# Optimization experiments

Hardware: AMD Instinct MI355X
Metric: run time of the kernel (lower is better)

## Reference

```python
import jax, jax.numpy as jnp
import numpy as np
import math

DIM = 384
HEADS = 12
WIN = (12, 12)
N = WIN[0] * WIN[1]  # 144
TABLE = (2 * WIN[0] - 1) * (2 * WIN[1] - 1)  # 529
B_ = 512
NW = 16
CPB_HIDDEN = 512


def setup_inputs() -> dict:
    key = jax.random.key(0)
    ks = jax.random.split(key, 12)
    x = jax.random.normal(ks[0], (B_, N, DIM), dtype=jnp.float32)
    relative_coords_table = jax.random.uniform(ks[1], (1, 2 * WIN[0] - 1, 2 * WIN[1] - 1, 2), dtype=jnp.float32) * 2.0 - 1.0
    relative_position_index = jax.random.randint(ks[2], (N, N), 0, TABLE, dtype=jnp.int64)
    mask = jnp.zeros((NW, N, N), dtype=jnp.float32)
    # learned params
    qkv_w = jax.random.normal(ks[3], (3 * DIM, DIM), dtype=jnp.float32) * (1.0 / math.sqrt(DIM))
    q_bias = jnp.zeros((DIM,), dtype=jnp.float32)
    k_bias = jnp.zeros((DIM,), dtype=jnp.float32)
    v_bias = jnp.zeros((DIM,), dtype=jnp.float32)
    logit_scale = jnp.full((HEADS, 1, 1), math.log(10.0), dtype=jnp.float32)
    cpb_w1 = jax.random.normal(ks[4], (CPB_HIDDEN, 2), dtype=jnp.float32) * 0.5
    cpb_b1 = jnp.zeros((CPB_HIDDEN,), dtype=jnp.float32)
    cpb_w2 = jax.random.normal(ks[5], (HEADS, CPB_HIDDEN), dtype=jnp.float32) * (1.0 / math.sqrt(CPB_HIDDEN))
    proj_w = jax.random.normal(ks[6], (DIM, DIM), dtype=jnp.float32) * (1.0 / math.sqrt(DIM))
    proj_b = jnp.zeros((DIM,), dtype=jnp.float32)
    return {
        'x': x,
        'relative_coords_table': relative_coords_table,
        'relative_position_index': relative_position_index,
        'mask': mask,
        'qkv_w': qkv_w, 'q_bias': q_bias, 'k_bias': k_bias, 'v_bias': v_bias,
        'logit_scale': logit_scale,
        'cpb_w1': cpb_w1, 'cpb_b1': cpb_b1, 'cpb_w2': cpb_w2,
        'proj_w': proj_w, 'proj_b': proj_b,
    }


def reference(x, relative_coords_table, relative_position_index, mask,
              qkv_w, q_bias, k_bias, v_bias, logit_scale,
              cpb_w1, cpb_b1, cpb_w2, proj_w, proj_b):
    Bw, n, C = x.shape
    H = HEADS
    d = C // H
    qkv_bias = jnp.concatenate([q_bias, k_bias, v_bias])
    qkv = x @ qkv_w.T + qkv_bias  # (Bw, n, 3C)
    qkv = qkv.reshape(Bw, n, 3, H, d).transpose(2, 0, 3, 1, 4)  # (3, Bw, H, n, d)
    q, k, v = qkv[0], qkv[1], qkv[2]
    # cosine attention
    qn = q / jnp.linalg.norm(q, axis=-1, keepdims=True)
    kn = k / jnp.linalg.norm(k, axis=-1, keepdims=True)
    attn = jnp.einsum('bhnd,bhmd->bhnm', qn, kn)
    scale = jnp.exp(jnp.minimum(logit_scale, math.log(1.0 / 0.01)))  # (H,1,1)
    attn = attn * scale[None]
    # CPB-MLP relative position bias
    h1 = jax.nn.relu(relative_coords_table @ cpb_w1.T + cpb_b1)  # (1,23,23,512)
    table = (h1 @ cpb_w2.T).reshape(-1, H)  # (529, H)
    rpb = table[relative_position_index.reshape(-1)].reshape(n, n, H)
    rpb = 16.0 * jax.nn.sigmoid(rpb.transpose(2, 0, 1))  # (H, n, n)
    attn = attn + rpb[None]
    # shifted-window mask
    nW = mask.shape[0]
    attn = attn.reshape(Bw // nW, nW, H, n, n) + mask[None, :, None]
    attn = attn.reshape(Bw, H, n, n)
    attn = jax.nn.softmax(attn, axis=-1)
    out = jnp.einsum('bhnm,bhmd->bhnd', attn, v)
    out = out.transpose(0, 2, 1, 3).reshape(Bw, n, C)
    out = out @ proj_w.T + proj_b
    return out
```

## Files before the change

kernel.cpp:

```cpp
#include <hip/hip_runtime.h>

#define DIMC 384
#define NHEADS 12
#define NTOK 144
#define TABLEN 529
#define BWIN 512
#define NWIN 16
#define CPBH 512

typedef unsigned short u16;
typedef unsigned int u32;
typedef __attribute__((ext_vector_type(8))) short short8;
typedef __attribute__((ext_vector_type(4))) float f32x4;

#define MFMA(a, b, c) __builtin_amdgcn_mfma_f32_16x16x32_bf16((a), (b), (c), 0, 0, 0)

__device__ __forceinline__ u16 f2bf(float f) {
  union { float f; u32 u; } v; v.f = f;
  u32 r = v.u + 0x7fffu + ((v.u >> 16) & 1u);
  return (u16)(r >> 16);
}
__device__ __forceinline__ u32 pk2(float a, float b) {
  return (u32)f2bf(a) | ((u32)f2bf(b) << 16);
}

__global__ __launch_bounds__(256) void cvt_bf16(const float* __restrict__ in,
                                                u16* __restrict__ out, int n8) {
  int i = blockIdx.x * 256 + threadIdx.x;
  if (i >= n8) return;
  const float4* p = (const float4*)(in + (size_t)i * 8);
  float4 a = p[0], b = p[1];
  uint4 r;
  r.x = pk2(a.x, a.y); r.y = pk2(a.z, a.w);
  r.z = pk2(b.x, b.y); r.w = pk2(b.z, b.w);
  *(uint4*)(out + (size_t)i * 8) = r;
}

__global__ void cpb_kernel(const float* __restrict__ rct,
                           const float* __restrict__ w1,
                           const float* __restrict__ b1,
                           const float* __restrict__ w2,
                           const float* __restrict__ logit_scale,
                           float* __restrict__ bias_tab,
                           float* __restrict__ scalev) {
  int t = blockIdx.x * blockDim.x + threadIdx.x;
  if (t < NHEADS) scalev[t] = __expf(fminf(logit_scale[t], 4.60517018598809f));
  if (t >= TABLEN * NHEADS) return;
  int i = t / NHEADS, h = t % NHEADS;
  float c0 = rct[2 * i], c1 = rct[2 * i + 1];
  const float* w2h = w2 + (size_t)h * CPBH;
  float acc = 0.f;
  for (int k = 0; k < CPBH; ++k) {
    float hv = fmaxf(0.f, fmaf(c0, w1[2 * k], fmaf(c1, w1[2 * k + 1], b1[k])));
    acc = fmaf(hv, w2h[k], acc);
  }
  bias_tab[i * NHEADS + h] = 16.f / (1.f + __expf(-acc));
}

__global__ __launch_bounds__(256) void cbias_kernel(const int* __restrict__ rpi,
                                                    const float* __restrict__ bias_tab,
                                                    const float* __restrict__ mask,
                                                    float* __restrict__ cb) {
  int e = blockIdx.x * 256 + threadIdx.x;
  if (e >= NWIN * NHEADS * NTOK * NTOK) return;
  int m = e % NTOK;
  int t = e / NTOK;
  int n = t % NTOK; t /= NTOK;
  int h = t % NHEADS;
  int w = t / NHEADS;
  cb[e] = bias_tab[rpi[n * NTOK + m] * NHEADS + h] + mask[(w * NTOK + n) * NTOK + m];
}

__global__ __launch_bounds__(576) void attn_fused(
    const u16* __restrict__ xb, const u16* __restrict__ wb,
    const float* __restrict__ q_bias, const float* __restrict__ k_bias,
    const float* __restrict__ v_bias, const float* __restrict__ cb,
    const float* __restrict__ scalev, u16* __restrict__ ctx) {
  __shared__ u16 smem[22656];
  u16* qn = smem;
  u16* kn = smem + 5760;
  u16* vT = smem + 11520;
  u16* Pc = smem + 16896;
  u16* xs = smem;
  u16* wsm = smem + 9216;

  int bid = blockIdx.x;
  int xcd = bid & 7;
  int i = bid >> 3;
  int wsub = i / 384;
  int j = i - wsub * 384;
  int bI = j / NHEADS;
  int h = j - bI * NHEADS;
  int w = xcd * 2 + wsub;
  int b = bI * NWIN + w;

  int tid = threadIdx.x;
  int lane = tid & 63, wv = tid >> 6;
  int g = lane >> 4, c = lane & 15;
  int rbase = wv * 16;

  f32x4 acc[6];
#pragma unroll
  for (int d = 0; d < 6; ++d) acc[d] = (f32x4){0.f, 0.f, 0.f, 0.f};

  int r4 = tid >> 2, b4 = tid & 3;
  bool hasW = tid < 384;
  int wrow = (r4 >> 5) * DIMC + h * 32 + (r4 & 31);
  int xwo0 = r4 * 64 + 8 * (b4 ^ (r4 & 7));
  int xwo1 = r4 * 64 + 8 * ((b4 + 4) ^ (r4 & 7));

  uint4 px, pw;
  px = *(const uint4*)(xb + ((size_t)b * NTOK + r4) * DIMC + b4 * 8);
  if (hasW) pw = *(const uint4*)(wb + (size_t)wrow * DIMC + b4 * 8);

  for (int t = 0; t < 12; ++t) {
    int xwo = (t & 1) ? xwo1 : xwo0;
    *(uint4*)(xs + xwo) = px;
    if (hasW) *(uint4*)(wsm + xwo) = pw;
    __syncthreads();
    if (t < 11) {
      int k0 = (t + 1) * 32;
      px = *(const uint4*)(xb + ((size_t)b * NTOK + r4) * DIMC + k0 + b4 * 8);
      if (hasW) pw = *(const uint4*)(wb + (size_t)wrow * DIMC + k0 + b4 * 8);
    }
    int par4 = (t & 1) * 4;
    int arow = rbase + c;
    short8 ax = *(const short8*)(xs + arow * 64 + 8 * ((g + par4) ^ (arow & 7)));
#pragma unroll
    for (int ni = 0; ni < 6; ++ni) {
      int row = ni * 16 + c;
      short8 bw = *(const short8*)(wsm + row * 64 + 8 * ((g + par4) ^ (row & 7)));
      acc[ni] = MFMA(ax, bw, acc[ni]);
    }
  }
  __syncthreads();

  float sch = scalev[h];
  float qb0 = q_bias[h * 32 + c], qb1 = q_bias[h * 32 + 16 + c];
  float kb0 = k_bias[h * 32 + c], kb1 = k_bias[h * 32 + 16 + c];
  float vb0 = v_bias[h * 32 + c], vb1 = v_bias[h * 32 + 16 + c];
#pragma unroll
  for (int r = 0; r < 4; ++r) {
    int row = rbase + g * 4 + r;
    float q0 = acc[0][r] + qb0, q1 = acc[1][r] + qb1;
    float ssq = q0 * q0 + q1 * q1;
    ssq += __shfl_xor(ssq, 1); ssq += __shfl_xor(ssq, 2);
    ssq += __shfl_xor(ssq, 4); ssq += __shfl_xor(ssq, 8);
    float siq = sch / sqrtf(ssq);
    qn[row * 40 + c] = f2bf(q0 * siq);
    qn[row * 40 + 16 + c] = f2bf(q1 * siq);
    float k0v = acc[2][r] + kb0, k1v = acc[3][r] + kb1;
    float ssk = k0v * k0v + k1v * k1v;
    ssk += __shfl_xor(ssk, 1); ssk += __shfl_xor(ssk, 2);
    ssk += __shfl_xor(ssk, 4); ssk += __shfl_xor(ssk, 8);
    float sik = 1.f / sqrtf(ssk);
    kn[row * 40 + c] = f2bf(k0v * sik);
    kn[row * 40 + 16 + c] = f2bf(k1v * sik);
    float v0 = acc[4][r] + vb0;
    float v1 = acc[5][r] + vb1;
    vT[c * 168 + row] = f2bf(v0);
    vT[(16 + c) * 168 + row] = f2bf(v1);
  }
  if (tid < 32) {
    uint4 z4 = {0u, 0u, 0u, 0u};
    *(uint4*)(vT + tid * 168 + 144) = z4;
    *(uint4*)(vT + tid * 168 + 152) = z4;
    *(uint4*)(vT + tid * 168 + 160) = z4;
  }
  __syncthreads();

  short8 aq = *(const short8*)(qn + (rbase + c) * 40 + g * 8);
  f32x4 S[9];
#pragma unroll
  for (int mt = 0; mt < 9; ++mt) {
    short8 bk = *(const short8*)(kn + (mt * 16 + c) * 40 + g * 8);
    f32x4 z = (f32x4){0.f, 0.f, 0.f, 0.f};
    S[mt] = MFMA(aq, bk, z);
  }

  const float* cbh = cb + (((size_t)w * NHEADS + h) * NTOK) * NTOK;
#pragma unroll
  for (int r = 0; r < 4; ++r) {
    int row = rbase + g * 4 + r;
    const float* crow = cbh + (size_t)row * NTOK + c;
    float sv[9];
    float mx = -1e30f;
#pragma unroll
    for (int mt = 0; mt < 9; ++mt) {
      float s = S[mt][r] + crow[mt * 16];
      sv[mt] = s;
      mx = fmaxf(mx, s);
    }
    mx = fmaxf(mx, __shfl_xor(mx, 1)); mx = fmaxf(mx, __shfl_xor(mx, 2));
    mx = fmaxf(mx, __shfl_xor(mx, 4)); mx = fmaxf(mx, __shfl_xor(mx, 8));
    float sum = 0.f;
#pragma unroll
    for (int mt = 0; mt < 9; ++mt) {
      float p = __expf(sv[mt] - mx);
      sv[mt] = p;
      sum += p;
    }
    sum += __shfl_xor(sum, 1); sum += __shfl_xor(sum, 2);
    sum += __shfl_xor(sum, 4); sum += __shfl_xor(sum, 8);
    float rinv = 1.f / sum;
#pragma unroll
    for (int mt = 0; mt < 9; ++mt) S[mt][r] = sv[mt] * rinv;
  }

  f32x4 po[2];
  po[0] = (f32x4){0.f, 0.f, 0.f, 0.f};
  po[1] = (f32x4){0.f, 0.f, 0.f, 0.f};
  for (int ck = 0; ck < 5; ++ck) {
#pragma unroll
    for (int mt2 = 0; mt2 < 2; ++mt2) {
      int MT = ck * 2 + mt2;
#pragma unroll
      for (int r = 0; r < 4; ++r) {
        int row = rbase + g * 4 + r;
        float p = (MT < 9) ? S[MT][r] : 0.f;
        Pc[row * 40 + mt2 * 16 + c] = f2bf(p);
      }
    }
    short8 pa = *(const short8*)(Pc + (rbase + c) * 40 + g * 8);
#pragma unroll
    for (int dt = 0; dt < 2; ++dt) {
      short8 vb = *(const short8*)(vT + (dt * 16 + c) * 168 + ck * 32 + g * 8);
      po[dt] = MFMA(pa, vb, po[dt]);
    }
  }

#pragma unroll
  for (int dt = 0; dt < 2; ++dt)
#pragma unroll
    for (int r = 0; r < 4; ++r) {
      int n = rbase + g * 4 + r;
      ctx[((size_t)b * NTOK + n) * DIMC + h * 32 + dt * 16 + c] = f2bf(po[dt][r]);
    }
}

__global__ __launch_bounds__(256) void proj_gemm(const u16* __restrict__ ctx,
                                                 const u16* __restrict__ pwb,
                                                 const float* __restrict__ proj_b,
                                                 float* __restrict__ out) {
  __shared__ u16 As[128 * 64];
  __shared__ u16 Bs[128 * 64];
  int bid = blockIdx.x;
  int nblk = bid % 3, mblk = bid / 3;
  size_t gm0 = (size_t)mblk * 128;
  int gn0 = nblk * 128;
  int tid = threadIdx.x, lane = tid & 63, wid = tid >> 6;
  int wr = wid >> 1, wc = wid & 1, g = lane >> 4, c = lane & 15;
  f32x4 acc[4][4];
#pragma unroll
  for (int i = 0; i < 4; ++i)
#pragma unroll
    for (int j = 0; j < 4; ++j) acc[i][j] = (f32x4){0.f, 0.f, 0.f, 0.f};

  for (int t = 0; t < 6; ++t) {
    int k0 = t * 64;
#pragma unroll
    for (int p = 0; p < 4; ++p) {
      int row = p * 32 + (tid >> 3);
      int seg = (tid & 7) * 8;
      uint4 va = *(const uint4*)(ctx + (gm0 + row) * DIMC + k0 + seg);
      *(uint4*)(As + row * 64 + seg) = va;
      uint4 vb = *(const uint4*)(pwb + (size_t)(gn0 + row) * DIMC + k0 + seg);
      *(uint4*)(Bs + row * 64 + seg) = vb;
    }
    __syncthreads();
#pragma unroll
    for (int kk = 0; kk < 64; kk += 32) {
      short8 a[4], bfr[4];
#pragma unroll
      for (int mi = 0; mi < 4; ++mi)
        a[mi] = *(const short8*)(As + (wr * 64 + mi * 16 + c) * 64 + kk + g * 8);
#pragma unroll
      for (int ni = 0; ni < 4; ++ni)
        bfr[ni] = *(const short8*)(Bs + (wc * 64 + ni * 16 + c) * 64 + kk + g * 8);
#pragma unroll
      for (int mi = 0; mi < 4; ++mi)
#pragma unroll
        for (int ni = 0; ni < 4; ++ni)
          acc[mi][ni] = MFMA(a[mi], bfr[ni], acc[mi][ni]);
    }
    __syncthreads();
  }
#pragma unroll
  for (int mi = 0; mi < 4; ++mi)
#pragma unroll
    for (int ni = 0; ni < 4; ++ni) {
      int gcol = gn0 + wc * 64 + ni * 16 + c;
      float bv = proj_b[gcol];
#pragma unroll
      for (int r = 0; r < 4; ++r) {
        size_t grow = gm0 + wr * 64 + mi * 16 + g * 4 + r;
        out[grow * DIMC + gcol] = acc[mi][ni][r] + bv;
      }
    }
}

extern "C" void kernel_launch(void* const* d_in, const int* in_sizes, int n_in,
                              void* d_out, int out_size, void* d_ws, size_t ws_size,
                              hipStream_t stream) {
  const float* x = (const float*)d_in[0];
  const float* rct = (const float*)d_in[1];
  const int* rpi = (const int*)d_in[2];
  const float* mask = (const float*)d_in[3];
  const float* qkv_w = (const float*)d_in[4];
  const float* q_bias = (const float*)d_in[5];
  const float* k_bias = (const float*)d_in[6];
  const float* v_bias = (const float*)d_in[7];
  const float* logit_scale = (const float*)d_in[8];
  const float* cpb_w1 = (const float*)d_in[9];
  const float* cpb_b1 = (const float*)d_in[10];
  const float* cpb_w2 = (const float*)d_in[11];
  const float* proj_w = (const float*)d_in[12];
  const float* proj_b = (const float*)d_in[13];
  float* out = (float*)d_out;

  char* ws = (char*)d_ws;
  size_t off = 0;
  auto alloc = [&](size_t bytes) {
    void* p = ws + off;
    off = (off + bytes + 255) & ~(size_t)255;
    return p;
  };
  const size_t NX = (size_t)BWIN * NTOK * DIMC;
  u16* xb = (u16*)alloc(NX * 2);
  u16* wqb = (u16*)alloc((size_t)3 * DIMC * DIMC * 2);
  u16* pwb = (u16*)alloc((size_t)DIMC * DIMC * 2);
  u16* ctx = (u16*)alloc(NX * 2);
  float* cbv = (float*)alloc((size_t)NWIN * NHEADS * NTOK * NTOK * 4);
  float* bias_tab = (float*)alloc((size_t)TABLEN * NHEADS * 4);
  float* scalev = (float*)alloc(64 * 4);

  cvt_bf16<<<(int)(NX / 8 + 255) / 256, 256, 0, stream>>>(x, xb, (int)(NX / 8));
  cvt_bf16<<<(3 * DIMC * DIMC / 8 + 255) / 256, 256, 0, stream>>>(qkv_w, wqb, 3 * DIMC * DIMC / 8);
  cvt_bf16<<<(DIMC * DIMC / 8 + 255) / 256, 256, 0, stream>>>(proj_w, pwb, DIMC * DIMC / 8);
  cpb_kernel<<<(TABLEN * NHEADS + 255) / 256, 256, 0, stream>>>(
      rct, cpb_w1, cpb_b1, cpb_w2, logit_scale, bias_tab, scalev);
  cbias_kernel<<<(NWIN * NHEADS * NTOK * NTOK + 255) / 256, 256, 0, stream>>>(
      rpi, bias_tab, mask, cbv);
  attn_fused<<<BWIN * NHEADS, 576, 0, stream>>>(
      xb, wqb, q_bias, k_bias, v_bias, cbv, scalev, ctx);
  proj_gemm<<<(BWIN * NTOK / 128) * 3, 256, 0, stream>>>(ctx, pwb, proj_b, out);
}
```

Before: 350.2 us.

## Process two heads per attention block to reuse loaded x tiles

Each attention block now computes the QKV projection for two heads at once, sharing each staged x tile across twice as many weight rows. The softmax attention for the two heads then runs sequentially inside the block. This halves the grid and cuts redundant x reads from global memory and L2. In exchange it raises accumulator register pressure, adds an extra barrier, and gives fewer, longer blocks.

```diff
diff --git a/kernel.cpp b/kernel.cpp
--- a/kernel.cpp
+++ b/kernel.cpp
@@ -87,155 +87,178 @@
   int bid = blockIdx.x;
   int xcd = bid & 7;
   int i = bid >> 3;
-  int wsub = i / 384;
-  int j = i - wsub * 384;
-  int bI = j / NHEADS;
-  int h = j - bI * NHEADS;
+  int wsub = i / 192;
+  int j = i - wsub * 192;
+  int bI = j / 6;
+  int hp = j - bI * 6;
   int w = xcd * 2 + wsub;
   int b = bI * NWIN + w;
+  int h0 = hp * 2;
 
   int tid = threadIdx.x;
   int lane = tid & 63, wv = tid >> 6;
   int g = lane >> 4, c = lane & 15;
   int rbase = wv * 16;
 
-  f32x4 acc[6];
-#pragma unroll
-  for (int d = 0; d < 6; ++d) acc[d] = (f32x4){0.f, 0.f, 0.f, 0.f};
+  f32x4 acc[2][6];
+#pragma unroll
+  for (int hh = 0; hh < 2; ++hh)
+#pragma unroll
+    for (int d = 0; d < 6; ++d) acc[hh][d] = (f32x4){0.f, 0.f, 0.f, 0.f};
 
   int r4 = tid >> 2, b4 = tid & 3;
-  bool hasW = tid < 384;
-  int wrow = (r4 >> 5) * DIMC + h * 32 + (r4 & 31);
-  int xwo0 = r4 * 64 + 8 * (b4 ^ (r4 & 7));
-  int xwo1 = r4 * 64 + 8 * ((b4 + 4) ^ (r4 & 7));
-
-  uint4 px, pw;
+  bool hasW1 = tid < 192;
+  int wr1 = 144 + r4;
+  int wg0 = (r4 >> 6) * DIMC + (h0 + ((r4 >> 5) & 1)) * 32 + (r4 & 31);
+  int wg1 = (wr1 >> 6) * DIMC + (h0 + ((wr1 >> 5) & 1)) * 32 + (wr1 & 31);
+  int xo0 = r4 * 64 + 8 * (b4 ^ (r4 & 7));
+  int xo1 = r4 * 64 + 8 * ((b4 + 4) ^ (r4 & 7));
+  int w1o0 = wr1 * 64 + 8 * (b4 ^ (wr1 & 7));
+  int w1o1 = wr1 * 64 + 8 * ((b4 + 4) ^ (wr1 & 7));
+
+  uint4 px, pw0, pw1;
   px = *(const uint4*)(xb + ((size_t)b * NTOK + r4) * DIMC + b4 * 8);
-  if (hasW) pw = *(const uint4*)(wb + (size_t)wrow * DIMC + b4 * 8);
+  pw0 = *(const uint4*)(wb + (size_t)wg0 * DIMC + b4 * 8);
+  if (hasW1) pw1 = *(const uint4*)(wb + (size_t)wg1 * DIMC + b4 * 8);
 
   for (int t = 0; t < 12; ++t) {
-    int xwo = (t & 1) ? xwo1 : xwo0;
-    *(uint4*)(xs + xwo) = px;
-    if (hasW) *(uint4*)(wsm + xwo) = pw;
+    if (t & 1) {
+      *(uint4*)(xs + xo1) = px;
+      *(uint4*)(wsm + xo1) = pw0;
+      if (hasW1) *(uint4*)(wsm + w1o1) = pw1;
+    } else {
+      *(uint4*)(xs + xo0) = px;
+      *(uint4*)(wsm + xo0) = pw0;
+      if (hasW1) *(uint4*)(wsm + w1o0) = pw1;
+    }
     __syncthreads();
     if (t < 11) {
       int k0 = (t + 1) * 32;
       px = *(const uint4*)(xb + ((size_t)b * NTOK + r4) * DIMC + k0 + b4 * 8);
-      if (hasW) pw = *(const uint4*)(wb + (size_t)wrow * DIMC + k0 + b4 * 8);
+      pw0 = *(const uint4*)(wb + (size_t)wg0 * DIMC + k0 + b4 * 8);
+      if (hasW1) pw1 = *(const uint4*)(wb + (size_t)wg1 * DIMC + k0 + b4 * 8);
     }
     int par4 = (t & 1) * 4;
     int arow = rbase + c;
     short8 ax = *(const short8*)(xs + arow * 64 + 8 * ((g + par4) ^ (arow & 7)));
 #pragma unroll
-    for (int ni = 0; ni < 6; ++ni) {
-      int row = ni * 16 + c;
-      short8 bw = *(const short8*)(wsm + row * 64 + 8 * ((g + par4) ^ (row & 7)));
-      acc[ni] = MFMA(ax, bw, acc[ni]);
-    }
+    for (int hh = 0; hh < 2; ++hh)
+#pragma unroll
+      for (int d = 0; d < 6; ++d) {
+        int row = (d >> 1) * 64 + hh * 32 + (d & 1) * 16 + c;
+        short8 bw = *(const short8*)(wsm + row * 64 + 8 * ((g + par4) ^ (row & 7)));
+        acc[hh][d] = MFMA(ax, bw, acc[hh][d]);
+      }
   }
   __syncthreads();
 
-  float sch = scalev[h];
-  float qb0 = q_bias[h * 32 + c], qb1 = q_bias[h * 32 + 16 + c];
-  float kb0 = k_bias[h * 32 + c], kb1 = k_bias[h * 32 + 16 + c];
-  float vb0 = v_bias[h * 32 + c], vb1 = v_bias[h * 32 + 16 + c];
-#pragma unroll
-  for (int r = 0; r < 4; ++r) {
-    int row = rbase + g * 4 + r;
-    float q0 = acc[0][r] + qb0, q1 = acc[1][r] + qb1;
-    float ssq = q0 * q0 + q1 * q1;
-    ssq += __shfl_xor(ssq, 1); ssq += __shfl_xor(ssq, 2);
-    ssq += __shfl_xor(ssq, 4); ssq += __shfl_xor(ssq, 8);
-    float siq = sch / sqrtf(ssq);
-    qn[row * 40 + c] = f2bf(q0 * siq);
-    qn[row * 40 + 16 + c] = f2bf(q1 * siq);
-    float k0v = acc[2][r] + kb0, k1v = acc[3][r] + kb1;
-    float ssk = k0v * k0v + k1v * k1v;
-    ssk += __shfl_xor(ssk, 1); ssk += __shfl_xor(ssk, 2);
-    ssk += __shfl_xor(ssk, 4); ssk += __shfl_xor(ssk, 8);
-    float sik = 1.f / sqrtf(ssk);
-    kn[row * 40 + c] = f2bf(k0v * sik);
-    kn[row * 40 + 16 + c] = f2bf(k1v * sik);
-    float v0 = acc[4][r] + vb0;
-    float v1 = acc[5][r] + vb1;
-    vT[c * 168 + row] = f2bf(v0);
-    vT[(16 + c) * 168 + row] = f2bf(v1);
+#pragma unroll
+  for (int hh = 0; hh < 2; ++hh) {
+    int h = h0 + hh;
+    if (hh) __syncthreads();
+
+    float sch = scalev[h];
+    float qb0 = q_bias[h * 32 + c], qb1 = q_bias[h * 32 + 16 + c];
+    float kb0 = k_bias[h * 32 + c], kb1 = k_bias[h * 32 + 16 + c];
+    float vb0 = v_bias[h * 32 + c], vb1 = v_bias[h * 32 + 16 + c];
+#pragma unroll
+    for (int r = 0; r < 4; ++r) {
+      int row = rbase + g * 4 + r;
+      float q0 = acc[hh][0][r] + qb0, q1 = acc[hh][1][r] + qb1;
+      float ssq = q0 * q0 + q1 * q1;
+      ssq += __shfl_xor(ssq, 1); ssq += __shfl_xor(ssq, 2);
+      ssq += __shfl_xor(ssq, 4); ssq += __shfl_xor(ssq, 8);
+      float siq = sch / sqrtf(ssq);
+      qn[row * 40 + c] = f2bf(q0 * siq);
+      qn[row * 40 + 16 + c] = f2bf(q1 * siq);
+      float k0v = acc[hh][2][r] + kb0, k1v = acc[hh][3][r] + kb1;
+      float ssk = k0v * k0v + k1v * k1v;
+      ssk += __shfl_xor(ssk, 1); ssk += __shfl_xor(ssk, 2);
+      ssk += __shfl_xor(ssk, 4); ssk += __shfl_xor(ssk, 8);
+      float sik = 1.f / sqrtf(ssk);
+      kn[row * 40 + c] = f2bf(k0v * sik);
+      kn[row * 40 + 16 + c] = f2bf(k1v * sik);
+      float v0 = acc[hh][4][r] + vb0;
+      float v1 = acc[hh][5][r] + vb1;
+      vT[c * 168 + row] = f2bf(v0);
+      vT[(16 + c) * 168 + row] = f2bf(v1);
+    }
+    if (hh == 0 && tid < 32) {
+      uint4 z4 = {0u, 0u, 0u, 0u};
+      *(uint4*)(vT + tid * 168 + 144) = z4;
+      *(uint4*)(vT + tid * 168 + 152) = z4;
+      *(uint4*)(vT + tid * 168 + 160) = z4;
+    }
+    __syncthreads();
+
+    short8 aq = *(const short8*)(qn + (rbase + c) * 40 + g * 8);
+    f32x4 S[9];
+#pragma unroll
+    for (int mt = 0; mt < 9; ++mt) {
+      short8 bk = *(const short8*)(kn + (mt * 16 + c) * 40 + g * 8);
+      f32x4 z = (f32x4){0.f, 0.f, 0.f, 0.f};
+      S[mt] = MFMA(aq, bk, z);
+    }
+
+    const float* cbh = cb + (((size_t)w * NHEADS + h) * NTOK) * NTOK;
+#pragma unroll
+    for (int r = 0; r < 4; ++r) {
+      int row = rbase + g * 4 + r;
+      const float* crow = cbh + (size_t)row * NTOK + c;
+      float sv[9];
+      float mx = -1e30f;
+#pragma unroll
+      for (int mt = 0; mt < 9; ++mt) {
+        float s = S[mt][r] + crow[mt * 16];
+        sv[mt] = s;
+        mx = fmaxf(mx, s);
+      }
+      mx = fmaxf(mx, __shfl_xor(mx, 1)); mx = fmaxf(mx, __shfl_xor(mx, 2));
+      mx = fmaxf(mx, __shfl_xor(mx, 4)); mx = fmaxf(mx, __shfl_xor(mx, 8));
+      float sum = 0.f;
+#pragma unroll
+      for (int mt = 0; mt < 9; ++mt) {
+        float p = __expf(sv[mt] - mx);
+        sv[mt] = p;
+        sum += p;
+      }
+      sum += __shfl_xor(sum, 1); sum += __shfl_xor(sum, 2);
+      sum += __shfl_xor(sum, 4); sum += __shfl_xor(sum, 8);
+      float rinv = 1.f / sum;
+#pragma unroll
+      for (int mt = 0; mt < 9; ++mt) S[mt][r] = sv[mt] * rinv;
+    }
+
+    f32x4 po[2];
+    po[0] = (f32x4){0.f, 0.f, 0.f, 0.f};
+    po[1] = (f32x4){0.f, 0.f, 0.f, 0.f};
+    for (int ck = 0; ck < 5; ++ck) {
+#pragma unroll
+      for (int mt2 = 0; mt2 < 2; ++mt2) {
+        int MT = ck * 2 + mt2;
+#pragma unroll
+        for (int r = 0; r < 4; ++r) {
+          int row = rbase + g * 4 + r;
+          float p = (MT < 9) ? S[MT][r] : 0.f;
+          Pc[row * 40 + mt2 * 16 + c] = f2bf(p);
+        }
+      }
+      short8 pa = *(const short8*)(Pc + (rbase + c) * 40 + g * 8);
+#pragma unroll
+      for (int dt = 0; dt < 2; ++dt) {
+        short8 vb = *(const short8*)(vT + (dt * 16 + c) * 168 + ck * 32 + g * 8);
+        po[dt] = MFMA(pa, vb, po[dt]);
+      }
+    }
+
+#pragma unroll
+    for (int dt = 0; dt < 2; ++dt)
+#pragma unroll
+      for (int r = 0; r < 4; ++r) {
+        int n = rbase + g * 4 + r;
+        ctx[((size_t)b * NTOK + n) * DIMC + h * 32 + dt * 16 + c] = f2bf(po[dt][r]);
+      }
   }
-  if (tid < 32) {
-    uint4 z4 = {0u, 0u, 0u, 0u};
-    *(uint4*)(vT + tid * 168 + 144) = z4;
-    *(uint4*)(vT + tid * 168 + 152) = z4;
-    *(uint4*)(vT + tid * 168 + 160) = z4;
-  }
-  __syncthreads();
-
-  short8 aq = *(const short8*)(qn + (rbase + c) * 40 + g * 8);
-  f32x4 S[9];
-#pragma unroll
-  for (int mt = 0; mt < 9; ++mt) {
-    short8 bk = *(const short8*)(kn + (mt * 16 + c) * 40 + g * 8);
-    f32x4 z = (f32x4){0.f, 0.f, 0.f, 0.f};
-    S[mt] = MFMA(aq, bk, z);
-  }
-
-  const float* cbh = cb + (((size_t)w * NHEADS + h) * NTOK) * NTOK;
-#pragma unroll
-  for (int r = 0; r < 4; ++r) {
-    int row = rbase + g * 4 + r;
-    const float* crow = cbh + (size_t)row * NTOK + c;
-    float sv[9];
-    float mx = -1e30f;
-#pragma unroll
-    for (int mt = 0; mt < 9; ++mt) {
-      float s = S[mt][r] + crow[mt * 16];
-      sv[mt] = s;
-      mx = fmaxf(mx, s);
-    }
-    mx = fmaxf(mx, __shfl_xor(mx, 1)); mx = fmaxf(mx, __shfl_xor(mx, 2));
-    mx = fmaxf(mx, __shfl_xor(mx, 4)); mx = fmaxf(mx, __shfl_xor(mx, 8));
-    float sum = 0.f;
-#pragma unroll
-    for (int mt = 0; mt < 9; ++mt) {
-      float p = __expf(sv[mt] - mx);
-      sv[mt] = p;
-      sum += p;
-    }
-    sum += __shfl_xor(sum, 1); sum += __shfl_xor(sum, 2);
-    sum += __shfl_xor(sum, 4); sum += __shfl_xor(sum, 8);
-    float rinv = 1.f / sum;
-#pragma unroll
-    for (int mt = 0; mt < 9; ++mt) S[mt][r] = sv[mt] * rinv;
-  }
-
-  f32x4 po[2];
-  po[0] = (f32x4){0.f, 0.f, 0.f, 0.f};
-  po[1] = (f32x4){0.f, 0.f, 0.f, 0.f};
-  for (int ck = 0; ck < 5; ++ck) {
-#pragma unroll
-    for (int mt2 = 0; mt2 < 2; ++mt2) {
-      int MT = ck * 2 + mt2;
-#pragma unroll
-      for (int r = 0; r < 4; ++r) {
-        int row = rbase + g * 4 + r;
-        float p = (MT < 9) ? S[MT][r] : 0.f;
-        Pc[row * 40 + mt2 * 16 + c] = f2bf(p);
-      }
-    }
-    short8 pa = *(const short8*)(Pc + (rbase + c) * 40 + g * 8);
-#pragma unroll
-    for (int dt = 0; dt < 2; ++dt) {
-      short8 vb = *(const short8*)(vT + (dt * 16 + c) * 168 + ck * 32 + g * 8);
-      po[dt] = MFMA(pa, vb, po[dt]);
-    }
-  }
-
-#pragma unroll
-  for (int dt = 0; dt < 2; ++dt)
-#pragma unroll
-    for (int r = 0; r < 4; ++r) {
-      int n = rbase + g * 4 + r;
-      ctx[((size_t)b * NTOK + n) * DIMC + h * 32 + dt * 16 + c] = f2bf(po[dt][r]);
-    }
 }
 
 __global__ __launch_bounds__(256) void proj_gemm(const u16* __restrict__ ctx,
@@ -341,7 +364,7 @@
       rct, cpb_w1, cpb_b1, cpb_w2, logit_scale, bias_tab, scalev);
   cbias_kernel<<<(NWIN * NHEADS * NTOK * NTOK + 255) / 256, 256, 0, stream>>>(
       rpi, bias_tab, mask, cbv);
-  attn_fused<<<BWIN * NHEADS, 576, 0, stream>>>(
+  attn_fused<<<BWIN * 6, 576, 0, stream>>>(
       xb, wqb, q_bias, k_bias, v_bias, cbv, scalev, ctx);
   proj_gemm<<<(BWIN * NTOK / 128) * 3, 256, 0, stream>>>(ctx, pwb, proj_b, out);
 }
```

New measurement: 352.3 us. Within noise of the previous version (+0.6%).
